# Kernel tuning notes

Hardware: AMD Instinct MI355X
Metric: run time of the kernel (lower is better)

## Reference

```python
import jax, jax.numpy as jnp
import numpy as np

HEADS = 4
K = 3  # neighborhood kernel size
EPS = 1e-5


def _nbr_idx(dim, k):
    # NATTEN semantics: window start clamped so the full k-window stays in-bounds.
    i = jnp.arange(dim)
    start = jnp.clip(i - k // 2, 0, dim - k)
    return start[:, None] + jnp.arange(k)[None, :]  # [dim, k]


def _gather_windows(t, ix, iy, iz):
    # t: [B, X, Y, Z, n, c] -> [B, X, Y, Z, K^3, n, c]
    t = t[:, ix]                 # [B, X, k, Y, Z, n, c]
    t = t[:, :, :, iy]           # [B, X, k, Y, k, Z, n, c]
    t = t[:, :, :, :, :, iz]     # [B, X, k, Y, k, Z, k, n, c]
    t = t.transpose(0, 1, 3, 5, 2, 4, 6, 7, 8)  # [B,X,Y,Z,k,k,k,n,c]
    B, X, Y, Z = t.shape[0], t.shape[1], t.shape[2], t.shape[3]
    return t.reshape(B, X, Y, Z, K * K * K, HEADS, -1)


def setup_inputs() -> dict:
    key = jax.random.key(0)
    k1, k2, k3 = jax.random.split(key, 3)
    C = 128
    x = jax.random.normal(k1, (1, C, 32, 32, 32), dtype=jnp.float32)
    ln_gamma = jnp.ones((C,), jnp.float32)
    ln_beta = jnp.zeros((C,), jnp.float32)
    qkv_w = jax.random.normal(k2, (3 * C, C), dtype=jnp.float32) * 0.02
    qkv_b = jnp.zeros((3 * C,), jnp.float32)
    proj_w = jax.random.normal(k3, (C, C), dtype=jnp.float32) * 0.02
    proj_b = jnp.zeros((C,), jnp.float32)
    return {"x": x, "ln_gamma": ln_gamma, "ln_beta": ln_beta,
            "qkv_w": qkv_w, "qkv_b": qkv_b, "proj_w": proj_w, "proj_b": proj_b}


def reference(x, ln_gamma, ln_beta, qkv_w, qkv_b, proj_w, proj_b):
    B, C, X, Y, Z = x.shape
    hd = C // HEADS
    scale = hd ** -0.5

    # permute to channels-last + LayerNorm over C
    h = x.transpose(0, 2, 3, 4, 1)  # [B,X,Y,Z,C]
    mu = jnp.mean(h, axis=-1, keepdims=True)
    var = jnp.mean(jnp.square(h - mu), axis=-1, keepdims=True)
    h = (h - mu) * jax.lax.rsqrt(var + EPS) * ln_gamma + ln_beta

    # QKV projection
    qkv = h @ qkv_w.T + qkv_b                     # [B,X,Y,Z,3C]
    q, k, v = jnp.split(qkv, 3, axis=-1)
    q = q.reshape(B, X, Y, Z, HEADS, hd)
    k = k.reshape(B, X, Y, Z, HEADS, hd)
    v = v.reshape(B, X, Y, Z, HEADS, hd)

    ix, iy, iz = _nbr_idx(X, K), _nbr_idx(Y, K), _nbr_idx(Z, K)
    k_win = _gather_windows(k, ix, iy, iz)  # [B,X,Y,Z,27,n,hd]
    v_win = _gather_windows(v, ix, iy, iz)

    attn = jnp.einsum('bxyznc,bxyzknc->bxyznk', q * scale, k_win)
    attn = jax.nn.softmax(attn, axis=-1)
    out = jnp.einsum('bxyznk,bxyzknc->bxyznc', attn, v_win)
    out = out.reshape(B, X, Y, Z, C)

    out = out @ proj_w.T + proj_b                 # output projection
    return out.transpose(0, 4, 1, 2, 3) + x      # residual, channels-first
```

## Files before the change

### kernel.cpp

```cpp
#include <hip/hip_runtime.h>

#define N_VOX 32768
#define CCH 128
#define EPSV 1e-5f

typedef __attribute__((ext_vector_type(8))) short bfrag;
typedef __attribute__((ext_vector_type(4))) float ffrag;
typedef __attribute__((ext_vector_type(2))) unsigned int u32x2;

__device__ __forceinline__ float bf2f(unsigned short u) {
    union { unsigned int i; float f; } c; c.i = ((unsigned int)u) << 16; return c.f;
}
__device__ __forceinline__ unsigned short f2bf(float f) {
    union { float f; unsigned int i; } c; c.f = f;
    unsigned int i = c.i;
    return (unsigned short)((i + 0x7FFFu + ((i >> 16) & 1u)) >> 16);
}
__device__ __forceinline__ unsigned int cvtpk(float lo, float hi) {
    unsigned int r;
    asm("v_cvt_pk_bf16_f32 %0, %1, %2" : "=v"(r) : "v"(lo), "v"(hi));
    return r;
}

__global__ __launch_bounds__(256) void ln_kernel(const float* __restrict__ x,
                                                 const float* __restrict__ gamma,
                                                 const float* __restrict__ beta,
                                                 unsigned short* __restrict__ h) {
    __shared__ float xs[128 * 65];
    __shared__ float g[128], b[128];
    __shared__ float ps[256], pq[256];
    __shared__ float muS[64], rsS[64];
    int t = threadIdx.x;
    int v0 = blockIdx.x * 64;
    if (t < 128) { g[t] = gamma[t]; b[t] = beta[t]; }
    int vv = t & 63, cq = t >> 6;
    for (int cb = 0; cb < 32; cb++) {
        int c = cb * 4 + cq;
        xs[c * 65 + vv] = x[(size_t)c * N_VOX + v0 + vv];
    }
    __syncthreads();
    float s = 0.f, sq = 0.f;
    for (int i = 0; i < 32; i++) {
        float val = xs[(cq * 32 + i) * 65 + vv];
        s += val; sq += val * val;
    }
    ps[t] = s; pq[t] = sq;
    __syncthreads();
    if (t < 64) {
        float S = ps[t] + ps[t + 64] + ps[t + 128] + ps[t + 192];
        float Q = pq[t] + pq[t + 64] + pq[t + 128] + pq[t + 192];
        float mu = S * (1.0f / 128.0f);
        float var = Q * (1.0f / 128.0f) - mu * mu;
        muS[t] = mu; rsS[t] = rsqrtf(var + EPSV);
    }
    __syncthreads();
    int c8 = t & 15;
    for (int pass = 0; pass < 4; pass++) {
        int v = pass * 16 + (t >> 4);
        float mu = muS[v], rs = rsS[v];
        float val[8];
        #pragma unroll
        for (int i = 0; i < 8; i++) {
            int c = c8 * 8 + i;
            val[i] = (xs[c * 65 + v] - mu) * rs * g[c] + b[c];
        }
        uint4 q;
        q.x = cvtpk(val[0], val[1]);
        q.y = cvtpk(val[2], val[3]);
        q.z = cvtpk(val[4], val[5]);
        q.w = cvtpk(val[6], val[7]);
        *(uint4*)&h[(size_t)(v0 + v) * 128 + c8 * 8] = q;
    }
}

__global__ __launch_bounds__(256) void qkv_gemm(const unsigned short* __restrict__ h,
                                                const float* __restrict__ w,
                                                const float* __restrict__ bias,
                                                unsigned short* __restrict__ qkv) {
    __shared__ __align__(16) unsigned short a_s[64 * 136];
    __shared__ __align__(16) unsigned short b_s[64 * 136];
    int t = threadIdx.x;
    int m0 = blockIdx.x * 64, o0 = blockIdx.y * 64;
    {
        int r4 = t >> 4, c8 = t & 15;
        #pragma unroll
        for (int pass = 0; pass < 4; pass++) {
            int r = pass * 16 + r4;
            *(uint4*)&a_s[r * 136 + c8 * 8] =
                *(const uint4*)&h[(size_t)(m0 + r) * 128 + c8 * 8];
            float4 w0 = *(const float4*)&w[(size_t)(o0 + r) * 128 + c8 * 8];
            float4 w1 = *(const float4*)&w[(size_t)(o0 + r) * 128 + c8 * 8 + 4];
            uint4 q;
            q.x = cvtpk(w0.x, w0.y);
            q.y = cvtpk(w0.z, w0.w);
            q.z = cvtpk(w1.x, w1.y);
            q.w = cvtpk(w1.z, w1.w);
            *(uint4*)&b_s[r * 136 + c8 * 8] = q;
        }
    }
    __syncthreads();
    int wvi = t >> 6, lane = t & 63, m = lane & 15, quad = lane >> 4;
    ffrag acc[4] = {ffrag{0,0,0,0}, ffrag{0,0,0,0}, ffrag{0,0,0,0}, ffrag{0,0,0,0}};
    #pragma unroll
    for (int kk = 0; kk < 4; kk++) {
        bfrag a = *(bfrag*)&a_s[(wvi * 16 + m) * 136 + kk * 32 + quad * 8];
        #pragma unroll
        for (int nt = 0; nt < 4; nt++) {
            bfrag bb = *(bfrag*)&b_s[(nt * 16 + m) * 136 + kk * 32 + quad * 8];
            acc[nt] = __builtin_amdgcn_mfma_f32_16x16x32_bf16(a, bb, acc[nt], 0, 0, 0);
        }
    }
    bool isq = (o0 < 128);
    #pragma unroll
    for (int nt = 0; nt < 4; nt++) {
        int o = o0 + nt * 16 + m;
        float bs = bias[o];
        int sec = o >> 7;
        int oc = o & 127;
        unsigned short* dst = qkv + (size_t)sec * ((size_t)N_VOX * 128);
        #pragma unroll
        for (int r = 0; r < 4; r++) {
            int vg = m0 + wvi * 16 + quad * 4 + r;
            float val = acc[nt][r] + bs;
            if (isq) val *= 0.17677669529663687f;
            dst[(size_t)vg * 128 + oc] = f2bf(val);
        }
    }
}

#define VT_STRIDE 100
__global__ __launch_bounds__(256) void attn_kernel(const unsigned short* __restrict__ qb,
                                                   const unsigned short* __restrict__ kb,
                                                   const unsigned short* __restrict__ vb,
                                                   unsigned short* __restrict__ ob) {
    __shared__ unsigned int vjtab[176];
    __shared__ __align__(16) unsigned short vt[4][32 * VT_STRIDE];

    int t = threadIdx.x;
    int bidx = blockIdx.x;
    int zh = bidx & 1, yy = (bidx >> 1) & 31, xx = bidx >> 6;
    int z0 = zh << 4;
    int sx = min(max(xx - 1, 0), 29);
    int sy = min(max(yy - 1, 0), 29);
    int zr0 = min(max(z0 - 1, 0), 14);
    int vox0 = (xx << 10) + (yy << 5) + z0;

    if (t < 176) {
        int r = t < 162 ? t : 161;
        int rxy = r / 18;
        int rzv = r - rxy * 18;
        int ax = rxy / 3;
        int by = rxy - ax * 3;
        vjtab[t] = (unsigned)(((sx + ax) << 10) + ((sy + by) << 5) + (zr0 + rzv));
    }
    __syncthreads();

    int wave = t >> 6, lane = t & 63;
    int hq = lane >> 4;
    int m = lane & 15;
    int ch0 = wave * 32;
    unsigned short* vts = &vt[wave][0];
    const int cp = m;

    #pragma unroll
    for (int u = 0; u < 6; u++) {
        int rb = u * 16 + hq * 4;
        unsigned int j0 = vjtab[rb + 0];
        unsigned int j1 = vjtab[rb + 1];
        unsigned int j2 = vjtab[rb + 2];
        unsigned int j3 = vjtab[rb + 3];
        unsigned int d0 = *(const unsigned int*)&vb[(size_t)j0 * 128 + ch0 + cp * 2];
        unsigned int d1 = *(const unsigned int*)&vb[(size_t)j1 * 128 + ch0 + cp * 2];
        unsigned int d2 = *(const unsigned int*)&vb[(size_t)j2 * 128 + ch0 + cp * 2];
        unsigned int d3 = *(const unsigned int*)&vb[(size_t)j3 * 128 + ch0 + cp * 2];
        unsigned int lo01 = __builtin_amdgcn_perm(d1, d0, 0x05040100u);
        unsigned int lo23 = __builtin_amdgcn_perm(d3, d2, 0x05040100u);
        unsigned int hi01 = __builtin_amdgcn_perm(d1, d0, 0x07060302u);
        unsigned int hi23 = __builtin_amdgcn_perm(d3, d2, 0x07060302u);
        u32x2 wlo; wlo.x = lo01; wlo.y = lo23;
        u32x2 whi; whi.x = hi01; whi.y = hi23;
        *(u32x2*)&vts[(2 * cp) * VT_STRIDE + rb] = wlo;
        *(u32x2*)&vts[(2 * cp + 1) * VT_STRIDE + rb] = whi;
    }

    bfrag qf = *(const bfrag*)&qb[(size_t)(vox0 + m) * 128 + ch0 + hq * 8];
    ffrag s[11];
    #pragma unroll
    for (int f = 0; f < 11; f++) {
        unsigned int vj = vjtab[f * 16 + m];
        bfrag kf = *(const bfrag*)&kb[(size_t)vj * 128 + ch0 + hq * 8];
        s[f] = __builtin_amdgcn_mfma_f32_16x16x32_bf16(kf, qf, ffrag{0,0,0,0}, 0, 0, 0);
    }

    int zv = z0 + m;
    int szv = min(max(zv - 1, 0), 29);
    unsigned int wz = (unsigned int)(szv - zr0);
    unsigned int rz = 4u * (unsigned int)hq;
    float mx = -1e30f;
    #pragma unroll
    for (int f = 0; f < 11; f++) {
        #pragma unroll
        for (int i = 0; i < 4; i++) {
            unsigned int ri = rz + (unsigned int)i;
            ri = min(ri, ri - 18u);
            bool valid = (ri - wz) <= 2u;
            if (f == 10) valid = valid && ((4 * hq + i) < 2);
            float sv = valid ? s[f][i] : -1e30f;
            s[f][i] = sv;
            mx = fmaxf(mx, sv);
        }
        rz = min(rz + 16u, rz - 2u);
    }
    mx = fmaxf(mx, __shfl_xor(mx, 16));
    mx = fmaxf(mx, __shfl_xor(mx, 32));
    float sum = 0.f;
    #pragma unroll
    for (int f = 0; f < 11; f++) {
        #pragma unroll
        for (int i = 0; i < 4; i++) {
            float p = __expf(s[f][i] - mx);
            s[f][i] = p;
            sum += p;
        }
    }
    sum += __shfl_xor(sum, 16);
    sum += __shfl_xor(sum, 32);
    float inv = 1.0f / sum;

    ffrag acc0 = ffrag{0,0,0,0};
    ffrag acc1 = ffrag{0,0,0,0};
    const unsigned short* ab = &vt[wave][m * VT_STRIDE + hq * 4];
    #pragma unroll
    for (int f = 0; f < 6; f++) {
        u32x2 pb; pb.x = cvtpk(s[f][0], s[f][1]); pb.y = cvtpk(s[f][2], s[f][3]);
        u32x2 av0 = *(const u32x2*)&ab[f * 16];
        u32x2 av1 = *(const u32x2*)&ab[16 * VT_STRIDE + f * 16];
        asm("v_mfma_f32_16x16x16_bf16 %0, %1, %2, %0" : "+v"(acc0) : "v"(av0), "v"(pb));
        asm("v_mfma_f32_16x16x16_bf16 %0, %1, %2, %0" : "+v"(acc1) : "v"(av1), "v"(pb));
    }

    #pragma unroll
    for (int u = 6; u < 11; u++) {
        int rb = u * 16 + hq * 4;
        unsigned int j0 = vjtab[rb + 0];
        unsigned int j1 = vjtab[rb + 1];
        unsigned int j2 = vjtab[rb + 2];
        unsigned int j3 = vjtab[rb + 3];
        unsigned int d0 = *(const unsigned int*)&vb[(size_t)j0 * 128 + ch0 + cp * 2];
        unsigned int d1 = *(const unsigned int*)&vb[(size_t)j1 * 128 + ch0 + cp * 2];
        unsigned int d2 = *(const unsigned int*)&vb[(size_t)j2 * 128 + ch0 + cp * 2];
        unsigned int d3 = *(const unsigned int*)&vb[(size_t)j3 * 128 + ch0 + cp * 2];
        if (u == 10) {
            if (rb + 0 >= 162) d0 = 0u;
            if (rb + 1 >= 162) d1 = 0u;
            if (rb + 2 >= 162) d2 = 0u;
            if (rb + 3 >= 162) d3 = 0u;
        }
        unsigned int lo01 = __builtin_amdgcn_perm(d1, d0, 0x05040100u);
        unsigned int lo23 = __builtin_amdgcn_perm(d3, d2, 0x05040100u);
        unsigned int hi01 = __builtin_amdgcn_perm(d1, d0, 0x07060302u);
        unsigned int hi23 = __builtin_amdgcn_perm(d3, d2, 0x07060302u);
        u32x2 wlo; wlo.x = lo01; wlo.y = lo23;
        u32x2 whi; whi.x = hi01; whi.y = hi23;
        int lc = rb - 96;
        *(u32x2*)&vts[(2 * cp) * VT_STRIDE + lc] = wlo;
        *(u32x2*)&vts[(2 * cp + 1) * VT_STRIDE + lc] = whi;
    }

    #pragma unroll
    for (int f = 6; f < 11; f++) {
        u32x2 pb; pb.x = cvtpk(s[f][0], s[f][1]); pb.y = cvtpk(s[f][2], s[f][3]);
        int lc = f * 16 - 96;
        u32x2 av0 = *(const u32x2*)&ab[lc];
        u32x2 av1 = *(const u32x2*)&ab[16 * VT_STRIDE + lc];
        asm("v_mfma_f32_16x16x16_bf16 %0, %1, %2, %0" : "+v"(acc0) : "v"(av0), "v"(pb));
        asm("v_mfma_f32_16x16x16_bf16 %0, %1, %2, %0" : "+v"(acc1) : "v"(av1), "v"(pb));
    }

    size_t obase = (size_t)(vox0 + m) * 128 + ch0 + hq * 4;
    {
        u32x2 ov;
        ov.x = cvtpk(acc0[0] * inv, acc0[1] * inv);
        ov.y = cvtpk(acc0[2] * inv, acc0[3] * inv);
        *(u32x2*)&ob[obase] = ov;
    }
    {
        u32x2 ov;
        ov.x = cvtpk(acc1[0] * inv, acc1[1] * inv);
        ov.y = cvtpk(acc1[2] * inv, acc1[3] * inv);
        *(u32x2*)&ob[obase + 16] = ov;
    }
}

__global__ __launch_bounds__(256) void proj_gemm(const unsigned short* __restrict__ a,
                                                 const float* __restrict__ w,
                                                 const float* __restrict__ bias,
                                                 const float* __restrict__ xres,
                                                 float* __restrict__ out) {
    __shared__ __align__(16) unsigned short a_s[64 * 136];
    __shared__ __align__(16) unsigned short b_s[64 * 136];
    int t = threadIdx.x;
    int m0 = blockIdx.x * 64, o0 = blockIdx.y * 64;
    {
        int r4 = t >> 4, c8 = t & 15;
        #pragma unroll
        for (int pass = 0; pass < 4; pass++) {
            int r = pass * 16 + r4;
            *(uint4*)&a_s[r * 136 + c8 * 8] =
                *(const uint4*)&a[(size_t)(m0 + r) * 128 + c8 * 8];
            float4 w0 = *(const float4*)&w[(size_t)(o0 + r) * 128 + c8 * 8];
            float4 w1 = *(const float4*)&w[(size_t)(o0 + r) * 128 + c8 * 8 + 4];
            uint4 q;
            q.x = cvtpk(w0.x, w0.y);
            q.y = cvtpk(w0.z, w0.w);
            q.z = cvtpk(w1.x, w1.y);
            q.w = cvtpk(w1.z, w1.w);
            *(uint4*)&b_s[r * 136 + c8 * 8] = q;
        }
    }
    __syncthreads();
    int wvi = t >> 6, lane = t & 63, m = lane & 15, quad = lane >> 4;
    ffrag acc[4] = {ffrag{0,0,0,0}, ffrag{0,0,0,0}, ffrag{0,0,0,0}, ffrag{0,0,0,0}};
    #pragma unroll
    for (int kk = 0; kk < 4; kk++) {
        bfrag av = *(bfrag*)&a_s[(wvi * 16 + m) * 136 + kk * 32 + quad * 8];
        #pragma unroll
        for (int nt = 0; nt < 4; nt++) {
            bfrag bb = *(bfrag*)&b_s[(nt * 16 + m) * 136 + kk * 32 + quad * 8];
            acc[nt] = __builtin_amdgcn_mfma_f32_16x16x32_bf16(av, bb, acc[nt], 0, 0, 0);
        }
    }
    #pragma unroll
    for (int nt = 0; nt < 4; nt++) {
        int o = o0 + nt * 16 + m;
        float bs = bias[o];
        int vg = m0 + wvi * 16 + quad * 4;
        float4 r = *(const float4*)&xres[(size_t)o * N_VOX + vg];
        float4 ov;
        ov.x = acc[nt][0] + bs + r.x;
        ov.y = acc[nt][1] + bs + r.y;
        ov.z = acc[nt][2] + bs + r.z;
        ov.w = acc[nt][3] + bs + r.w;
        *(float4*)&out[(size_t)o * N_VOX + vg] = ov;
    }
}

extern "C" void kernel_launch(void* const* d_in, const int* in_sizes, int n_in,
                              void* d_out, int out_size, void* d_ws, size_t ws_size,
                              hipStream_t stream) {
    const float* x      = (const float*)d_in[0];
    const float* gamma  = (const float*)d_in[1];
    const float* beta   = (const float*)d_in[2];
    const float* qkv_w  = (const float*)d_in[3];
    const float* qkv_b  = (const float*)d_in[4];
    const float* proj_w = (const float*)d_in[5];
    const float* proj_b = (const float*)d_in[6];
    float* out = (float*)d_out;

    unsigned short* h    = (unsigned short*)d_ws;
    unsigned short* qkv  = (unsigned short*)((char*)d_ws + (8u << 20));
    unsigned short* attn = h;

    hipLaunchKernelGGL(ln_kernel, dim3(512), dim3(256), 0, stream, x, gamma, beta, h);
    hipLaunchKernelGGL(qkv_gemm, dim3(512, 6), dim3(256), 0, stream, h, qkv_w, qkv_b, qkv);
    const unsigned short* qb = qkv;
    const unsigned short* kb = qkv + (size_t)N_VOX * 128;
    const unsigned short* vb = qkv + (size_t)2 * N_VOX * 128;
    hipLaunchKernelGGL(attn_kernel, dim3(2048), dim3(256), 0, stream, qb, kb, vb, attn);
    hipLaunchKernelGGL(proj_gemm, dim3(512, 2), dim3(256), 0, stream, attn, proj_w, proj_b, x, out);
}
```

Measured before the change: 129.5 us.

## Stage all V rows in LDS upfront and swizzle block order for locality

The V-transpose staging now covers all 176 neighborhood rows in one pass before the QK MFMAs, replacing the two-phase reuse of a 100-stride LDS buffer. This removes the mid-kernel second gather and lets every V load be issued early, overlapping with the score computation. The block index is also remapped so that consecutive hardware blocks are spread across eight interleaved groups, which changes L2/cache locality across XCDs. The cost is LDS per block rising from about 25KB to about 48KB, which can lower occupancy.

Result: faster. 119.8 us (-7.5%).

```diff
diff --git a/kernel.cpp b/kernel.cpp
--- a/kernel.cpp
+++ b/kernel.cpp
@@ -128,7 +128,7 @@
     }
 }
 
-#define VT_STRIDE 100
+#define VT_STRIDE 188
 __global__ __launch_bounds__(256) void attn_kernel(const unsigned short* __restrict__ qb,
                                                    const unsigned short* __restrict__ kb,
                                                    const unsigned short* __restrict__ vb,
@@ -137,7 +137,8 @@
     __shared__ __align__(16) unsigned short vt[4][32 * VT_STRIDE];
 
     int t = threadIdx.x;
-    int bidx = blockIdx.x;
+    int hw = blockIdx.x;
+    int bidx = (hw & 7) * 256 + (hw >> 3);
     int zh = bidx & 1, yy = (bidx >> 1) & 31, xx = bidx >> 6;
     int z0 = zh << 4;
     int sx = min(max(xx - 1, 0), 29);
@@ -159,28 +160,36 @@
     int hq = lane >> 4;
     int m = lane & 15;
     int ch0 = wave * 32;
+
     unsigned short* vts = &vt[wave][0];
-    const int cp = m;
-
-    #pragma unroll
-    for (int u = 0; u < 6; u++) {
-        int rb = u * 16 + hq * 4;
-        unsigned int j0 = vjtab[rb + 0];
-        unsigned int j1 = vjtab[rb + 1];
-        unsigned int j2 = vjtab[rb + 2];
-        unsigned int j3 = vjtab[rb + 3];
-        unsigned int d0 = *(const unsigned int*)&vb[(size_t)j0 * 128 + ch0 + cp * 2];
-        unsigned int d1 = *(const unsigned int*)&vb[(size_t)j1 * 128 + ch0 + cp * 2];
-        unsigned int d2 = *(const unsigned int*)&vb[(size_t)j2 * 128 + ch0 + cp * 2];
-        unsigned int d3 = *(const unsigned int*)&vb[(size_t)j3 * 128 + ch0 + cp * 2];
-        unsigned int lo01 = __builtin_amdgcn_perm(d1, d0, 0x05040100u);
-        unsigned int lo23 = __builtin_amdgcn_perm(d3, d2, 0x05040100u);
-        unsigned int hi01 = __builtin_amdgcn_perm(d1, d0, 0x07060302u);
-        unsigned int hi23 = __builtin_amdgcn_perm(d3, d2, 0x07060302u);
-        u32x2 wlo; wlo.x = lo01; wlo.y = lo23;
-        u32x2 whi; whi.x = hi01; whi.y = hi23;
-        *(u32x2*)&vts[(2 * cp) * VT_STRIDE + rb] = wlo;
-        *(u32x2*)&vts[(2 * cp + 1) * VT_STRIDE + rb] = whi;
+    {
+        const int cp = m;
+        #pragma unroll
+        for (int u = 0; u < 11; u++) {
+            int rb = u * 16 + hq * 4;
+            unsigned int j0 = vjtab[rb + 0];
+            unsigned int j1 = vjtab[rb + 1];
+            unsigned int j2 = vjtab[rb + 2];
+            unsigned int j3 = vjtab[rb + 3];
+            unsigned int d0 = *(const unsigned int*)&vb[(size_t)j0 * 128 + ch0 + cp * 2];
+            unsigned int d1 = *(const unsigned int*)&vb[(size_t)j1 * 128 + ch0 + cp * 2];
+            unsigned int d2 = *(const unsigned int*)&vb[(size_t)j2 * 128 + ch0 + cp * 2];
+            unsigned int d3 = *(const unsigned int*)&vb[(size_t)j3 * 128 + ch0 + cp * 2];
+            if (u == 10) {
+                if (rb + 0 >= 162) d0 = 0u;
+                if (rb + 1 >= 162) d1 = 0u;
+                if (rb + 2 >= 162) d2 = 0u;
+                if (rb + 3 >= 162) d3 = 0u;
+            }
+            unsigned int lo01 = __builtin_amdgcn_perm(d1, d0, 0x05040100u);
+            unsigned int lo23 = __builtin_amdgcn_perm(d3, d2, 0x05040100u);
+            unsigned int hi01 = __builtin_amdgcn_perm(d1, d0, 0x07060302u);
+            unsigned int hi23 = __builtin_amdgcn_perm(d3, d2, 0x07060302u);
+            u32x2 wlo; wlo.x = lo01; wlo.y = lo23;
+            u32x2 whi; whi.x = hi01; whi.y = hi23;
+            *(u32x2*)&vts[(2 * cp) * VT_STRIDE + rb] = wlo;
+            *(u32x2*)&vts[(2 * cp + 1) * VT_STRIDE + rb] = whi;
+        }
     }
 
     bfrag qf = *(const bfrag*)&qb[(size_t)(vox0 + m) * 128 + ch0 + hq * 8];
@@ -231,48 +240,10 @@
     ffrag acc1 = ffrag{0,0,0,0};
     const unsigned short* ab = &vt[wave][m * VT_STRIDE + hq * 4];
     #pragma unroll
-    for (int f = 0; f < 6; f++) {
+    for (int f = 0; f < 11; f++) {
         u32x2 pb; pb.x = cvtpk(s[f][0], s[f][1]); pb.y = cvtpk(s[f][2], s[f][3]);
         u32x2 av0 = *(const u32x2*)&ab[f * 16];
         u32x2 av1 = *(const u32x2*)&ab[16 * VT_STRIDE + f * 16];
-        asm("v_mfma_f32_16x16x16_bf16 %0, %1, %2, %0" : "+v"(acc0) : "v"(av0), "v"(pb));
-        asm("v_mfma_f32_16x16x16_bf16 %0, %1, %2, %0" : "+v"(acc1) : "v"(av1), "v"(pb));
-    }
-
-    #pragma unroll
-    for (int u = 6; u < 11; u++) {
-        int rb = u * 16 + hq * 4;
-        unsigned int j0 = vjtab[rb + 0];
-        unsigned int j1 = vjtab[rb + 1];
-        unsigned int j2 = vjtab[rb + 2];
-        unsigned int j3 = vjtab[rb + 3];
-        unsigned int d0 = *(const unsigned int*)&vb[(size_t)j0 * 128 + ch0 + cp * 2];
-        unsigned int d1 = *(const unsigned int*)&vb[(size_t)j1 * 128 + ch0 + cp * 2];
-        unsigned int d2 = *(const unsigned int*)&vb[(size_t)j2 * 128 + ch0 + cp * 2];
-        unsigned int d3 = *(const unsigned int*)&vb[(size_t)j3 * 128 + ch0 + cp * 2];
-        if (u == 10) {
-            if (rb + 0 >= 162) d0 = 0u;
-            if (rb + 1 >= 162) d1 = 0u;
-            if (rb + 2 >= 162) d2 = 0u;
-            if (rb + 3 >= 162) d3 = 0u;
-        }
-        unsigned int lo01 = __builtin_amdgcn_perm(d1, d0, 0x05040100u);
-        unsigned int lo23 = __builtin_amdgcn_perm(d3, d2, 0x05040100u);
-        unsigned int hi01 = __builtin_amdgcn_perm(d1, d0, 0x07060302u);
-        unsigned int hi23 = __builtin_amdgcn_perm(d3, d2, 0x07060302u);
-        u32x2 wlo; wlo.x = lo01; wlo.y = lo23;
-        u32x2 whi; whi.x = hi01; whi.y = hi23;
-        int lc = rb - 96;
-        *(u32x2*)&vts[(2 * cp) * VT_STRIDE + lc] = wlo;
-        *(u32x2*)&vts[(2 * cp + 1) * VT_STRIDE + lc] = whi;
-    }
-
-    #pragma unroll
-    for (int f = 6; f < 11; f++) {
-        u32x2 pb; pb.x = cvtpk(s[f][0], s[f][1]); pb.y = cvtpk(s[f][2], s[f][3]);
-        int lc = f * 16 - 96;
-        u32x2 av0 = *(const u32x2*)&ab[lc];
-        u32x2 av1 = *(const u32x2*)&ab[16 * VT_STRIDE + lc];
         asm("v_mfma_f32_16x16x16_bf16 %0, %1, %2, %0" : "+v"(acc0) : "v"(av0), "v"(pb));
         asm("v_mfma_f32_16x16x16_bf16 %0, %1, %2, %0" : "+v"(acc1) : "v"(av1), "v"(pb));
     }
```
